# Performance work log

Hardware: AMD Instinct MI355X
Metric: run time of the kernel (lower is better)

Reference implementation:

```python
import jax, jax.numpy as jnp
import numpy as np

EPS = 1e-6

def _layernorm(x, gamma, beta):
    mu = jnp.mean(x, axis=-1, keepdims=True)
    var = jnp.mean(jnp.square(x - mu), axis=-1, keepdims=True)
    return (x - mu) * jax.lax.rsqrt(var + EPS) * gamma + beta


def setup_inputs() -> dict:
    key = jax.random.key(0)
    ks = jax.random.split(key, 8)
    B, N, C, F = 2, 2048, 1024, 4096
    s = 0.02
    return {
        "x": jax.random.normal(ks[0], (B, N, C), jnp.float32),
        "Wq": jax.random.normal(ks[1], (C, C), jnp.float32) * s,
        "Wk": jax.random.normal(ks[2], (C, C), jnp.float32) * s,
        "Wv": jax.random.normal(ks[3], (C, C), jnp.float32) * s,
        "Wp": jax.random.normal(ks[4], (C, C), jnp.float32) * s,
        "bp": jnp.zeros((C,), jnp.float32),
        "W1": jax.random.normal(ks[5], (C, F), jnp.float32) * s,
        "b1": jnp.zeros((F,), jnp.float32),
        "W2": jax.random.normal(ks[6], (F, C), jnp.float32) * s,
        "b2": jnp.zeros((C,), jnp.float32),
        "gamma1": jnp.ones((C,), jnp.float32),
        "beta1": jnp.zeros((C,), jnp.float32),
        "gamma2": jnp.ones((C,), jnp.float32),
        "beta2": jnp.zeros((C,), jnp.float32),
    }


def reference(x, Wq, Wk, Wv, Wp, bp, W1, b1, W2, b2, gamma1, beta1, gamma2, beta2):
    B, N, C = x.shape
    H = 16
    D = C // H
    scale = D ** -0.5

    xn = _layernorm(x, gamma1, beta1)
    # QKV projections (no bias); q pre-scaled by head_dim**-0.5 as in source
    q = (xn @ Wq * scale).reshape(B, N, H, D).transpose(0, 2, 1, 3)  # bhnd
    k = (xn @ Wk).reshape(B, N, H, D).transpose(0, 2, 1, 3)
    v = (xn @ Wv).reshape(B, N, H, D).transpose(0, 2, 1, 3)

    attn = jax.nn.softmax(jnp.einsum("bhnd,bhmd->bhnm", q, k), axis=-1)
    y = jnp.einsum("bhnm,bhmd->bhnd", attn, v)
    y = y.transpose(0, 2, 1, 3).reshape(B, N, C)
    x = x + (y @ Wp + bp)

    xn2 = _layernorm(x, gamma2, beta2)
    h = jax.nn.gelu(xn2 @ W1 + b1, approximate=False)  # keras 'gelu' is exact
    x = x + (h @ W2 + b2)
    return x
```

## Files before the change

kernel.cpp:

```cpp
#include <hip/hip_runtime.h>
#include <math.h>

#define BN  4096
#define SEQ 2048
#define CH  1024
#define FF  4096
#define NH  16
#define HD  64

typedef short bf16x8 __attribute__((ext_vector_type(8)));
typedef float f32x4  __attribute__((ext_vector_type(4)));

#define MFMA16(a,b,c) __builtin_amdgcn_mfma_f32_16x16x32_bf16(a,b,c,0,0,0)

__device__ __forceinline__ unsigned short f2b(float f){
  unsigned u = __float_as_uint(f);
  u += 0x7fffu + ((u>>16)&1u);
  return (unsigned short)(u>>16);
}

__device__ __forceinline__ unsigned pk2(float a, float b){
  return __builtin_amdgcn_perm(__float_as_uint(b), __float_as_uint(a), 0x07060302u);
}

#if __has_builtin(__builtin_amdgcn_exp2f)
__device__ __forceinline__ float fexp2(float x){ return __builtin_amdgcn_exp2f(x); }
#else
__device__ __forceinline__ float fexp2(float x){
  float r; asm("v_exp_f32 %0, %1" : "=v"(r) : "v"(x)); return r;
}
#endif

__device__ __forceinline__ void gl2lds16(const void* g, void* l){
  __builtin_amdgcn_global_load_lds(
      (__attribute__((address_space(1))) void*)g,
      (__attribute__((address_space(3))) void*)l, 16, 0, 0);
}

__global__ __launch_bounds__(256) void transpose_cvt(const float* __restrict__ in,
    unsigned short* __restrict__ out, int R, int S, float scale)
{
  __shared__ float tile[64][65];
  const int tid = threadIdx.x;
  const int tx = tid & 63, ty = tid >> 6;
  const int s0 = blockIdx.x * 64, r0 = blockIdx.y * 64;
  #pragma unroll
  for (int j = 0; j < 16; j++){
    int r = ty + j*4;
    tile[r][tx] = in[(size_t)(r0 + r)*S + s0 + tx];
  }
  __syncthreads();
  #pragma unroll
  for (int j = 0; j < 16; j++){
    int s = ty + j*4;
    out[(size_t)(s0 + s)*R + r0 + tx] = f2b(tile[tx][s] * scale);
  }
}

__global__ __launch_bounds__(256) void ln_kernel(const float* __restrict__ x,
    const float* __restrict__ gamma, const float* __restrict__ beta,
    unsigned short* __restrict__ out)
{
  const int row = blockIdx.x, tid = threadIdx.x;
  const float4 xv = ((const float4*)(x + (size_t)row*CH))[tid];
  float s  = xv.x + xv.y + xv.z + xv.w;
  float ss = xv.x*xv.x + xv.y*xv.y + xv.z*xv.z + xv.w*xv.w;
  #pragma unroll
  for (int off = 1; off < 64; off <<= 1){
    s  += __shfl_xor(s,  off, 64);
    ss += __shfl_xor(ss, off, 64);
  }
  __shared__ float red[8];
  const int w = tid >> 6;
  if ((tid & 63) == 0){ red[w] = s; red[4+w] = ss; }
  __syncthreads();
  s  = red[0]+red[1]+red[2]+red[3];
  ss = red[4]+red[5]+red[6]+red[7];
  const float mu   = s * (1.f/CH);
  const float rstd = rsqrtf(ss*(1.f/CH) - mu*mu + 1e-6f);
  const float4 g = ((const float4*)gamma)[tid];
  const float4 b = ((const float4*)beta )[tid];
  ushort4 o;
  o.x = f2b((xv.x-mu)*rstd*g.x + b.x);
  o.y = f2b((xv.y-mu)*rstd*g.y + b.y);
  o.z = f2b((xv.z-mu)*rstd*g.z + b.z);
  o.w = f2b((xv.w-mu)*rstd*g.w + b.w);
  ((ushort4*)(out + (size_t)row*CH))[tid] = o;
}

template<int BNT,int BIAS,int GELU,int RES,int OMODE,int SPLITK>
__global__ __launch_bounds__(256,2) void gemm_bt(const unsigned short* __restrict__ A,
    const unsigned short* __restrict__ Bt, const float* __restrict__ bias,
    const float* __restrict__ resid, float* __restrict__ outF,
    unsigned short* __restrict__ outB, unsigned short* __restrict__ outK,
    unsigned short* __restrict__ outV, int M, int Nn, int K)
{
  constexpr int MI = (BNT==128) ? 4 : 2;
  constexpr int BCH = (BNT==128) ? 4 : 2;
  __shared__ __align__(16) unsigned short Al[128*64];
  __shared__ __align__(16) unsigned short Bl[BNT*64];
  const int tid = threadIdx.x;
  const int w = tid >> 6, lane = tid & 63;
  const int quad = lane >> 4, l16 = lane & 15;
  const int m0 = blockIdx.y*128, n0 = blockIdx.x*BNT;
  const int wm = (BNT==128) ? (w >> 1)*64 : w*32;
  const int wn = (BNT==128) ? (w & 1)*64 : 0;
  const int srow = lane >> 3, sslot = lane & 7;
  f32x4 acc[MI][4] = {};
  const int kseg = SPLITK > 1 ? K / SPLITK : K;
  const int kBeg = SPLITK > 1 ? blockIdx.z * kseg : 0;
  for (int k0 = kBeg; k0 < kBeg + kseg; k0 += 64){
    __syncthreads();
    #pragma unroll
    for (int i = 0; i < 4; i++){
      const int rb = (w*4 + i)*8;
      const int r = rb + srow;
      const int c = sslot ^ (r & 7);
      gl2lds16(A + (size_t)(m0 + r)*K + k0 + c*8, (char*)Al + rb*128);
    }
    #pragma unroll
    for (int i = 0; i < BCH; i++){
      const int rb = (w*BCH + i)*8;
      const int r = rb + srow;
      const int c = sslot ^ (r & 7);
      gl2lds16(Bt + (size_t)(n0 + r)*K + k0 + c*8, (char*)Bl + rb*128);
    }
    __syncthreads();
    #pragma unroll
    for (int kc = 0; kc < 2; kc++){
      bf16x8 af[MI], bfr[4];
      #pragma unroll
      for (int mi = 0; mi < MI; mi++){
        const int r = wm + mi*16 + l16;
        af[mi] = *(const bf16x8*)(Al + r*64 + (((kc*4 + quad) ^ (r & 7))*8));
      }
      #pragma unroll
      for (int nj = 0; nj < 4; nj++){
        const int r = wn + nj*16 + l16;
        bfr[nj] = *(const bf16x8*)(Bl + r*64 + (((kc*4 + quad) ^ (r & 7))*8));
      }
      #pragma unroll
      for (int mi = 0; mi < MI; mi++)
        #pragma unroll
        for (int nj = 0; nj < 4; nj++)
          acc[mi][nj] = MFMA16(af[mi], bfr[nj], acc[mi][nj]);
    }
  }
  #pragma unroll
  for (int nj = 0; nj < 4; nj++){
    const int col = n0 + wn + nj*16 + l16;
    const float bv = BIAS ? bias[col] : 0.f;
    #pragma unroll
    for (int mi = 0; mi < MI; mi++){
      #pragma unroll
      for (int r = 0; r < 4; r++){
        const int row = m0 + wm + mi*16 + quad*4 + r;
        float v = acc[mi][nj][r];
        if (SPLITK > 1){
          if (blockIdx.z == 0){
            if (BIAS) v += bias[col];
            if (RES)  v += resid[(size_t)row*Nn + col];
          }
          atomicAdd(&outF[(size_t)row*Nn + col], v);
          continue;
        }
        v += bv;
        if (GELU) v = 0.5f*v*(1.f + erff(v*0.70710678118654752f));
        if (RES)  v += resid[(size_t)row*Nn + col];
        if (OMODE == 0) outF[(size_t)row*Nn + col] = v;
        else if (OMODE == 1) outB[(size_t)row*Nn + col] = f2b(v);
        else {
          const int cg = col >> 10, c = col & (CH-1);
          if (cg == 0)      outB[(size_t)row*CH + c] = f2b(v);
          else if (cg == 1) outK[(size_t)row*CH + c] = f2b(v);
          else {
            const int bb = row >> 11, n = row & (SEQ-1);
            const int hh = c >> 6,  d = c & (HD-1);
            const int np = (n & ~63) | (((n & 15) << 2) | ((n >> 4) & 3));
            outV[((size_t)((bb*NH + hh)*HD + d))*SEQ + np] = f2b(v);
          }
        }
      }
    }
  }
}

__global__ __launch_bounds__(256,2) void attn_kernel(const unsigned short* __restrict__ q,
    const unsigned short* __restrict__ k, const unsigned short* __restrict__ vt,
    unsigned short* __restrict__ y)
{
  __shared__ __align__(16) unsigned short Kl[2][64*64];
  __shared__ __align__(16) unsigned short Vl[2][64*64];
  __shared__ __align__(16) unsigned short Pp[4][64*68];
  const int tid = threadIdx.x;
  const int w = tid >> 6, lane = tid & 63;
  const int wq = w & 1, wk = w >> 1;
  const int quad = lane >> 4, l16 = lane & 15;
  const int bh = blockIdx.y;
  const int b = bh >> 4, h = bh & 15;
  const size_t tb  = ((size_t)b*SEQ)*CH + h*HD;
  const size_t vb_ = (size_t)bh*HD*SEQ;
  const int qr0 = blockIdx.x*128 + wq*64;

  bf16x8 qf[4][2];
  #pragma unroll
  for (int mi = 0; mi < 4; mi++)
    #pragma unroll
    for (int kc = 0; kc < 2; kc++)
      qf[mi][kc] = *(const bf16x8*)(q + tb + (size_t)(qr0 + mi*16 + l16)*CH + kc*32 + quad*8);

  float sacc[4][4];
  f32x4 o[4][4] = {};
  #pragma unroll
  for (int mi = 0; mi < 4; mi++)
    #pragma unroll
    for (int r = 0; r < 4; r++) sacc[mi][r] = 0.f;

  for (int t = 0; t < 16; t++){
    const int kv0 = wk*1024 + t*64;
    __syncthreads();
    #pragma unroll
    for (int i = 0; i < 8; i++){
      const int r = i*8 + (lane >> 3);
      const int c = (lane & 7) ^ (r & 7);
      if (wq == 0)
        gl2lds16(k  + tb  + (size_t)(kv0 + r)*CH + c*8, (char*)&Kl[wk][0] + i*1024);
      else
        gl2lds16(vt + vb_ + (size_t)r*SEQ + kv0 + c*8, (char*)&Vl[wk][0] + i*1024);
    }
    __syncthreads();

    f32x4 s[4][4] = {};
    #pragma unroll
    for (int kc = 0; kc < 2; kc++){
      #pragma unroll
      for (int nj = 0; nj < 4; nj++){
        bf16x8 kf = *(const bf16x8*)(&Kl[wk][0] + (nj*16 + l16)*64 + (((kc*4 + quad) ^ (l16 & 7))*8));
        #pragma unroll
        for (int mi = 0; mi < 4; mi++)
          s[mi][nj] = MFMA16(qf[mi][kc], kf, s[mi][nj]);
      }
    }
    #pragma unroll
    for (int mi = 0; mi < 4; mi++){
      #pragma unroll
      for (int r = 0; r < 4; r++){
        const float p0 = fexp2(s[mi][0][r]);
        const float p1 = fexp2(s[mi][1][r]);
        const float p2 = fexp2(s[mi][2][r]);
        const float p3 = fexp2(s[mi][3][r]);
        sacc[mi][r] += (p0 + p1) + (p2 + p3);
        uint2 pk;
        pk.x = pk2(p0, p1);
        pk.y = pk2(p2, p3);
        const int prow = mi*16 + quad*4 + r;
        *(uint2*)(&Pp[w][prow*68 + l16*4]) = pk;
      }
    }
    #pragma unroll
    for (int kc = 0; kc < 2; kc++){
      bf16x8 pa[4];
      #pragma unroll
      for (int mi = 0; mi < 4; mi++)
        pa[mi] = *(const bf16x8*)(&Pp[w][(mi*16 + l16)*68 + kc*32 + quad*8]);
      #pragma unroll
      for (int nd = 0; nd < 4; nd++){
        bf16x8 vf = *(const bf16x8*)(&Vl[wk][0] + (nd*16 + l16)*64 + (((kc*4 + quad) ^ (l16 & 7))*8));
        #pragma unroll
        for (int mi = 0; mi < 4; mi++)
          o[mi][nd] = MFMA16(pa[mi], vf, o[mi][nd]);
      }
    }
  }

  __syncthreads();
  float* ob = wq ? (float*)&Vl[0][0] : (float*)&Kl[0][0];
  float* sb = (float*)&Pp[2 + wq][0];
  if (wk == 1){
    #pragma unroll
    for (int mi = 0; mi < 4; mi++)
      #pragma unroll
      for (int nd = 0; nd < 4; nd++)
        #pragma unroll
        for (int r = 0; r < 4; r++){
          const int idx = (mi*4 + nd)*4 + r;
          ob[lane*64 + ((idx + lane) & 63)] = o[mi][nd][r];
        }
    #pragma unroll
    for (int mi = 0; mi < 4; mi++)
      #pragma unroll
      for (int r = 0; r < 4; r++)
        sb[lane*16 + ((mi*4 + r + lane) & 15)] = sacc[mi][r];
  }
  __syncthreads();
  if (wk == 0){
    #pragma unroll
    for (int mi = 0; mi < 4; mi++)
      #pragma unroll
      for (int nd = 0; nd < 4; nd++)
        #pragma unroll
        for (int r = 0; r < 4; r++){
          const int idx = (mi*4 + nd)*4 + r;
          o[mi][nd][r] += ob[lane*64 + ((idx + lane) & 63)];
        }
    #pragma unroll
    for (int mi = 0; mi < 4; mi++){
      #pragma unroll
      for (int r = 0; r < 4; r++){
        float sum = sacc[mi][r] + sb[lane*16 + ((mi*4 + r + lane) & 15)];
        #pragma unroll
        for (int off = 1; off < 16; off <<= 1) sum += __shfl_xor(sum, off, 64);
        const float inv = 1.f / sum;
        const int qr = qr0 + mi*16 + quad*4 + r;
        #pragma unroll
        for (int nd = 0; nd < 4; nd++)
          y[tb + (size_t)qr*CH + nd*16 + l16] = f2b(o[mi][nd][r]*inv);
      }
    }
  }
}

extern "C" void kernel_launch(void* const* d_in, const int* in_sizes, int n_in,
                              void* d_out, int out_size, void* d_ws, size_t ws_size,
                              hipStream_t stream)
{
  (void)in_sizes; (void)n_in; (void)out_size; (void)ws_size;
  const float* x   = (const float*)d_in[0];
  const float* Wq  = (const float*)d_in[1];
  const float* Wk  = (const float*)d_in[2];
  const float* Wv  = (const float*)d_in[3];
  const float* Wp  = (const float*)d_in[4];
  const float* bp  = (const float*)d_in[5];
  const float* W1  = (const float*)d_in[6];
  const float* b1  = (const float*)d_in[7];
  const float* W2  = (const float*)d_in[8];
  const float* b2  = (const float*)d_in[9];
  const float* g1  = (const float*)d_in[10];
  const float* be1 = (const float*)d_in[11];
  const float* g2  = (const float*)d_in[12];
  const float* be2 = (const float*)d_in[13];
  float* out = (float*)d_out;
  char* ws = (char*)d_ws;
  const size_t MB = 1024*1024;
  unsigned short* wq_t = (unsigned short*)(ws +  0*MB);
  unsigned short* wk_t = (unsigned short*)(ws +  2*MB);
  unsigned short* wv_t = (unsigned short*)(ws +  4*MB);
  unsigned short* wp_t = (unsigned short*)(ws +  6*MB);
  unsigned short* w1_t = (unsigned short*)(ws +  8*MB);
  unsigned short* w2_t = (unsigned short*)(ws + 16*MB);
  unsigned short* xn   = (unsigned short*)(ws + 24*MB);
  unsigned short* qb   = (unsigned short*)(ws + 32*MB);
  unsigned short* kb   = (unsigned short*)(ws + 40*MB);
  unsigned short* vtb  = (unsigned short*)(ws + 48*MB);
  unsigned short* yb   = (unsigned short*)(ws + 56*MB);
  float*          x2   = (float*)         (ws + 64*MB);
  unsigned short* xn2  = (unsigned short*)(ws + 80*MB);
  unsigned short* hb   = (unsigned short*)(ws + 88*MB);

  transpose_cvt<<<dim3(16,16),256,0,stream>>>(Wq, wq_t, CH, CH, 0.18033688011112042f);
  transpose_cvt<<<dim3(16,16),256,0,stream>>>(Wk, wk_t, CH, CH, 1.f);
  transpose_cvt<<<dim3(16,16),256,0,stream>>>(Wv, wv_t, CH, CH, 1.f);
  transpose_cvt<<<dim3(16,16),256,0,stream>>>(Wp, wp_t, CH, CH, 1.f);
  transpose_cvt<<<dim3(64,16),256,0,stream>>>(W1, w1_t, CH, FF, 1.f);
  transpose_cvt<<<dim3(16,64),256,0,stream>>>(W2, w2_t, FF, CH, 1.f);

  ln_kernel<<<BN,256,0,stream>>>(x, g1, be1, xn);
  gemm_bt<128,0,0,0,3,0><<<dim3(24,32),256,0,stream>>>(xn, wq_t, nullptr, nullptr,
      nullptr, qb, kb, vtb, BN, 3072, CH);
  attn_kernel<<<dim3(16,32),256,0,stream>>>(qb, kb, vtb, yb);
  gemm_bt<64,1,0,1,0,0><<<dim3(16,32),256,0,stream>>>(yb, wp_t, bp, x, x2,
      nullptr, nullptr, nullptr, BN, CH, CH);
  ln_kernel<<<BN,256,0,stream>>>(x2, g2, be2, xn2);
  gemm_bt<128,1,1,0,1,0><<<dim3(32,32),256,0,stream>>>(xn2, w1_t, b1, nullptr, nullptr,
      hb, nullptr, nullptr, BN, FF, CH);
  hipMemsetAsync(out, 0, (size_t)BN*CH*sizeof(float), stream);
  gemm_bt<64,1,0,1,0,2><<<dim3(16,32,2),256,0,stream>>>(hb, w2_t, b2, x2, out,
      nullptr, nullptr, nullptr, BN, CH, FF);
}
```

Measured before the change: 373.4 us.

## Remap GEMM blocks per XCD for L2 reuse and merge weight transposes

GEMM launches switch from a 2D/3D grid to a flat 1D grid. Block IDs are remapped so that each XCD (id mod 8) owns a contiguous slice of N columns, which should keep B-tile reuse within one XCD's L2. The six weight transpose launches are merged into one kernel to cut launch overhead. The final split-K FFN2 GEMM moves from 64-wide to 128-wide N tiles with a matching grid of 512 blocks. Risks are tail imbalance and the assumption that blocks are dispatched round-robin across 8 XCDs.

```diff
diff --git a/kernel.cpp b/kernel.cpp
--- a/kernel.cpp
+++ b/kernel.cpp
@@ -37,13 +37,34 @@
       (__attribute__((address_space(3))) void*)l, 16, 0, 0);
 }
 
-__global__ __launch_bounds__(256) void transpose_cvt(const float* __restrict__ in,
-    unsigned short* __restrict__ out, int R, int S, float scale)
+__global__ __launch_bounds__(256) void transpose_all(
+    const float* __restrict__ Wq, const float* __restrict__ Wk,
+    const float* __restrict__ Wv, const float* __restrict__ Wp,
+    const float* __restrict__ W1, const float* __restrict__ W2,
+    unsigned short* __restrict__ wq_t, unsigned short* __restrict__ wk_t,
+    unsigned short* __restrict__ wv_t, unsigned short* __restrict__ wp_t,
+    unsigned short* __restrict__ w1_t, unsigned short* __restrict__ w2_t)
 {
+  const int id = blockIdx.x;
+  const float* in; unsigned short* out; int R, S, bx, by; float scale = 1.f;
+  if (id < 1024){
+    const int which = id >> 8, sub = id & 255;
+    R = CH; S = CH; bx = sub & 15; by = sub >> 4;
+    if (which == 0){ in = Wq; out = wq_t; scale = 0.18033688011112042f; }
+    else if (which == 1){ in = Wk; out = wk_t; }
+    else if (which == 2){ in = Wv; out = wv_t; }
+    else               { in = Wp; out = wp_t; }
+  } else if (id < 2048){
+    const int sub = id - 1024; in = W1; out = w1_t; R = CH; S = FF;
+    bx = sub & 63; by = sub >> 6;
+  } else {
+    const int sub = id - 2048; in = W2; out = w2_t; R = FF; S = CH;
+    bx = sub & 15; by = sub >> 4;
+  }
   __shared__ float tile[64][65];
   const int tid = threadIdx.x;
   const int tx = tid & 63, ty = tid >> 6;
-  const int s0 = blockIdx.x * 64, r0 = blockIdx.y * 64;
+  const int s0 = bx * 64, r0 = by * 64;
   #pragma unroll
   for (int j = 0; j < 16; j++){
     int r = ty + j*4;
@@ -88,7 +109,7 @@
   ((ushort4*)(out + (size_t)row*CH))[tid] = o;
 }
 
-template<int BNT,int BIAS,int GELU,int RES,int OMODE,int SPLITK>
+template<int BNT,int NB,int BIAS,int GELU,int RES,int OMODE,int SPLITK>
 __global__ __launch_bounds__(256,2) void gemm_bt(const unsigned short* __restrict__ A,
     const unsigned short* __restrict__ Bt, const float* __restrict__ bias,
     const float* __restrict__ resid, float* __restrict__ outF,
@@ -97,18 +118,26 @@
 {
   constexpr int MI = (BNT==128) ? 4 : 2;
   constexpr int BCH = (BNT==128) ? 4 : 2;
+  constexpr int Z  = (SPLITK > 1) ? SPLITK : 1;
+  constexpr int NT = NB / 8;
   __shared__ __align__(16) unsigned short Al[128*64];
   __shared__ __align__(16) unsigned short Bl[BNT*64];
   const int tid = threadIdx.x;
   const int w = tid >> 6, lane = tid & 63;
   const int quad = lane >> 4, l16 = lane & 15;
-  const int m0 = blockIdx.y*128, n0 = blockIdx.x*BNT;
+  const int flat = blockIdx.x;
+  const int xcd = flat & 7;
+  const int local = flat >> 3;
+  const int n_loc = local % NT;
+  const int z = (local / NT) % Z;
+  const int mstr = local / (NT * Z);
+  const int m0 = mstr * 128, n0 = (xcd * NT + n_loc) * BNT;
   const int wm = (BNT==128) ? (w >> 1)*64 : w*32;
   const int wn = (BNT==128) ? (w & 1)*64 : 0;
   const int srow = lane >> 3, sslot = lane & 7;
   f32x4 acc[MI][4] = {};
-  const int kseg = SPLITK > 1 ? K / SPLITK : K;
-  const int kBeg = SPLITK > 1 ? blockIdx.z * kseg : 0;
+  const int kseg = K / Z;
+  const int kBeg = z * kseg;
   for (int k0 = kBeg; k0 < kBeg + kseg; k0 += 64){
     __syncthreads();
     #pragma unroll
@@ -157,7 +186,7 @@
         const int row = m0 + wm + mi*16 + quad*4 + r;
         float v = acc[mi][nj][r];
         if (SPLITK > 1){
-          if (blockIdx.z == 0){
+          if (z == 0){
             if (BIAS) v += bias[col];
             if (RES)  v += resid[(size_t)row*Nn + col];
           }
@@ -357,23 +386,19 @@
   unsigned short* xn2  = (unsigned short*)(ws + 80*MB);
   unsigned short* hb   = (unsigned short*)(ws + 88*MB);
 
-  transpose_cvt<<<dim3(16,16),256,0,stream>>>(Wq, wq_t, CH, CH, 0.18033688011112042f);
-  transpose_cvt<<<dim3(16,16),256,0,stream>>>(Wk, wk_t, CH, CH, 1.f);
-  transpose_cvt<<<dim3(16,16),256,0,stream>>>(Wv, wv_t, CH, CH, 1.f);
-  transpose_cvt<<<dim3(16,16),256,0,stream>>>(Wp, wp_t, CH, CH, 1.f);
-  transpose_cvt<<<dim3(64,16),256,0,stream>>>(W1, w1_t, CH, FF, 1.f);
-  transpose_cvt<<<dim3(16,64),256,0,stream>>>(W2, w2_t, FF, CH, 1.f);
+  transpose_all<<<3072,256,0,stream>>>(Wq, Wk, Wv, Wp, W1, W2,
+                                       wq_t, wk_t, wv_t, wp_t, w1_t, w2_t);
 
   ln_kernel<<<BN,256,0,stream>>>(x, g1, be1, xn);
-  gemm_bt<128,0,0,0,3,0><<<dim3(24,32),256,0,stream>>>(xn, wq_t, nullptr, nullptr,
+  gemm_bt<128,24,0,0,0,3,0><<<768,256,0,stream>>>(xn, wq_t, nullptr, nullptr,
       nullptr, qb, kb, vtb, BN, 3072, CH);
   attn_kernel<<<dim3(16,32),256,0,stream>>>(qb, kb, vtb, yb);
-  gemm_bt<64,1,0,1,0,0><<<dim3(16,32),256,0,stream>>>(yb, wp_t, bp, x, x2,
+  gemm_bt<64,16,1,0,1,0,0><<<512,256,0,stream>>>(yb, wp_t, bp, x, x2,
       nullptr, nullptr, nullptr, BN, CH, CH);
   ln_kernel<<<BN,256,0,stream>>>(x2, g2, be2, xn2);
-  gemm_bt<128,1,1,0,1,0><<<dim3(32,32),256,0,stream>>>(xn2, w1_t, b1, nullptr, nullptr,
+  gemm_bt<128,32,1,1,0,1,0><<<1024,256,0,stream>>>(xn2, w1_t, b1, nullptr, nullptr,
       hb, nullptr, nullptr, BN, FF, CH);
   hipMemsetAsync(out, 0, (size_t)BN*CH*sizeof(float), stream);
-  gemm_bt<64,1,0,1,0,2><<<dim3(16,32,2),256,0,stream>>>(hb, w2_t, b2, x2, out,
+  gemm_bt<128,8,1,0,1,0,2><<<512,256,0,stream>>>(hb, w2_t, b2, x2, out,
       nullptr, nullptr, nullptr, BN, CH, FF);
 }
```

New measurement: 388.1 us. 1.04x slower.
